# Optimization experiments

Hardware: AMD Instinct MI355X
Metric: run time of the kernel (lower is better)

## Reference

```python
import jax, jax.numpy as jnp
import numpy as np
from jax import lax

B, S, H, W = 16, 5, 64, 64
D, DS, DEPTH, EXPAND, NC = 128, 16, 2, 2, 2


def _ln(x, w, b, eps=1e-5):
    m = x.mean(-1, keepdims=True)
    v = ((x - m) ** 2).mean(-1, keepdims=True)
    return (x - m) / jnp.sqrt(v + eps) * w + b


def _conv2d(x, w, b, stride, pad):
    y = lax.conv_general_dilated(x, w, (stride, stride), [(pad, pad), (pad, pad)],
                                 dimension_numbers=('NCHW', 'OIHW', 'NCHW'))
    return y + b[None, :, None, None]


def _convT2d(x, w, b):
    # torch ConvTranspose2d(k=4, s=2, p=1); w: (Cin, Cout, 4, 4)
    k = jnp.transpose(w[:, :, ::-1, ::-1], (1, 0, 2, 3))
    y = lax.conv_general_dilated(x, k, (1, 1), [(2, 2), (2, 2)], lhs_dilation=(2, 2),
                                 dimension_numbers=('NCHW', 'OIHW', 'NCHW'))
    return y + b[None, :, None, None]


def _dwconv1d(x, w, b):
    # x: [B, L, D]; torch depthwise Conv1d k=4 pad=3 then truncate to L == left-pad 3
    y = lax.conv_general_dilated(x.transpose(0, 2, 1), w, (1,), [(3, 0)],
                                 feature_group_count=w.shape[0],
                                 dimension_numbers=('NCH', 'OIH', 'NCH'))
    return (y + b[None, :, None]).transpose(0, 2, 1)


def _selective_scan(x, ln_w, ln_b, in_w, in_b, x_w, x_b, A_log, Dm, out_w, out_b):
    xn = _ln(x, ln_w, ln_b)
    xz = xn @ in_w.T + in_b
    xp, z = jnp.split(xz, 2, axis=-1)
    xp = jax.nn.silu(xp)
    z = jax.nn.sigmoid(z)
    u = xp @ x_w.T + x_b                        # [B, L, DS]
    a = jnp.exp(-jnp.exp(A_log))[0, 0]          # [DS] decay factor exp(A), A = -exp(A_log)

    def step(h, u_t):
        h = a * h + u_t
        return h, h

    _, hs = lax.scan(step, jnp.zeros((x.shape[0], DS), x.dtype), u.transpose(1, 0, 2))
    hs = hs.transpose(1, 0, 2)                  # [B, L, DS]
    y = (hs @ Dm) * z
    y = y @ out_w.T + out_b                     # dropout is identity at inference
    return x + y


def setup_inputs() -> dict:
    key = jax.random.key(0)
    ks = iter(jax.random.split(key, 64))

    def nrm(shape, scale=0.02):
        return (jax.random.normal(next(ks), shape) * scale).astype(jnp.float32)

    d, ds, hw = D, DS, H * W
    return {
        'x': jax.random.normal(next(ks), (B, S, H, W), dtype=jnp.float32),
        'emb_w': nrm((d, 1, 3, 3), 0.1), 'emb_b': jnp.zeros((d,), jnp.float32),
        'pos_embed': nrm((hw, d)), 'time_embed': nrm((S, d)),
        'blk_ln1_w': jnp.ones((DEPTH, d), jnp.float32), 'blk_ln1_b': jnp.zeros((DEPTH, d), jnp.float32),
        'blk_conv_w': nrm((DEPTH, d, 1, 4), 0.2), 'blk_conv_b': jnp.zeros((DEPTH, d), jnp.float32),
        'blk_sln_w': jnp.ones((DEPTH, d), jnp.float32), 'blk_sln_b': jnp.zeros((DEPTH, d), jnp.float32),
        'blk_A_log': nrm((DEPTH, 1, 1, ds), 0.5),
        'blk_D': nrm((DEPTH, ds, d), 0.1),
        'blk_in_w': nrm((DEPTH, 2 * d, d), 0.05), 'blk_in_b': jnp.zeros((DEPTH, 2 * d), jnp.float32),
        'blk_x_w': nrm((DEPTH, ds, d), 0.05), 'blk_x_b': jnp.zeros((DEPTH, ds), jnp.float32),
        'blk_out_w': nrm((DEPTH, d, d), 0.05), 'blk_out_b': jnp.zeros((DEPTH, d), jnp.float32),
        'blk_ln2_w': jnp.ones((DEPTH, d), jnp.float32), 'blk_ln2_b': jnp.zeros((DEPTH, d), jnp.float32),
        'blk_mlp_w1': nrm((DEPTH, EXPAND * d, d), 0.05), 'blk_mlp_b1': jnp.zeros((DEPTH, EXPAND * d), jnp.float32),
        'blk_mlp_w2': nrm((DEPTH, d, EXPAND * d), 0.05), 'blk_mlp_b2': jnp.zeros((DEPTH, d), jnp.float32),
        'down1_w': nrm((d, d, 3, 3), 0.05), 'down1_b': jnp.zeros((d,), jnp.float32),
        'down2_w': nrm((2 * d, d, 3, 3), 0.05), 'down2_b': jnp.zeros((2 * d,), jnp.float32),
        'bott_w': nrm((2 * d, 2 * d, 3, 3), 0.05), 'bott_b': jnp.zeros((2 * d,), jnp.float32),
        'up1_w': nrm((2 * d, d, 4, 4), 0.05), 'up1_b': jnp.zeros((d,), jnp.float32),
        'up2_w': nrm((2 * d, d, 4, 4), 0.05), 'up2_b': jnp.zeros((d,), jnp.float32),
        'final_w': nrm((NC, 2 * d, 1, 1), 0.05), 'final_b': jnp.zeros((NC,), jnp.float32),
    }


def reference(x, emb_w, emb_b, pos_embed, time_embed,
              blk_ln1_w, blk_ln1_b, blk_conv_w, blk_conv_b,
              blk_sln_w, blk_sln_b, blk_A_log, blk_D,
              blk_in_w, blk_in_b, blk_x_w, blk_x_b, blk_out_w, blk_out_b,
              blk_ln2_w, blk_ln2_b, blk_mlp_w1, blk_mlp_b1, blk_mlp_w2, blk_mlp_b2,
              down1_w, down1_b, down2_w, down2_b, bott_w, bott_b,
              up1_w, up1_b, up2_w, up2_b, final_w, final_b):
    b, s, h, w = x.shape
    # embed all frames at once (linear combination weights: 0.5 each, last frame 1.0)
    e = _conv2d(x.reshape(b * s, 1, h, w), emb_w, emb_b, 1, 1)      # [B*S, D, H, W]
    e = e.reshape(b, s, D, h * w).transpose(0, 1, 3, 2)              # [B, S, HW, D]
    e = e + pos_embed[None, None] + time_embed[:s][None, :, None, :]
    wts = jnp.where(jnp.arange(s) == s - 1, 1.0, 0.5).astype(x.dtype)
    emb = jnp.einsum('bsld,s->bld', e, wts)                          # [B, HW, D]
    for i in range(DEPTH):
        xn = _ln(emb, blk_ln1_w[i], blk_ln1_b[i])
        emb = emb + _dwconv1d(xn, blk_conv_w[i], blk_conv_b[i])
        emb = _selective_scan(emb, blk_sln_w[i], blk_sln_b[i], blk_in_w[i], blk_in_b[i],
                              blk_x_w[i], blk_x_b[i], blk_A_log[i], blk_D[i],
                              blk_out_w[i], blk_out_b[i])
        m = _ln(emb, blk_ln2_w[i], blk_ln2_b[i])
        m = jax.nn.gelu(m @ blk_mlp_w1[i].T + blk_mlp_b1[i], approximate=False)
        emb = emb + (m @ blk_mlp_w2[i].T + blk_mlp_b2[i])
    sp = emb.transpose(0, 2, 1).reshape(b, D, h, w)
    x1 = jax.nn.relu(_conv2d(sp, down1_w, down1_b, 2, 1))
    x2 = jax.nn.relu(_conv2d(x1, down2_w, down2_b, 2, 1))
    x2 = jax.nn.relu(_conv2d(x2, bott_w, bott_b, 1, 1))
    u1 = jax.nn.relu(_convT2d(x2, up1_w, up1_b))
    u1 = jnp.concatenate([u1, x1], axis=1)
    u2 = jax.nn.relu(_convT2d(u1, up2_w, up2_b))
    u2 = jnp.concatenate([u2, sp], axis=1)
    return _conv2d(u2, final_w, final_b, 1, 0)
```

## Files before the change

### kernel.cpp

```cpp
#include <hip/hip_runtime.h>
#include <cmath>

namespace {
constexpr int Bn = 16, Ln = 4096, Dn = 128, DSn = 16;
constexpr int Mtok = Bn * Ln;
constexpr int SLS = 138;
}

typedef short bfx8 __attribute__((ext_vector_type(8)));
typedef float f32x4 __attribute__((ext_vector_type(4)));

static __device__ __forceinline__ ushort f2bf(float f) {
  union { float f; unsigned u; } v; v.f = f;
  unsigned r = v.u + 0x7fff + ((v.u >> 16) & 1);
  return (ushort)(r >> 16);
}
static __device__ __forceinline__ float bf2f(ushort u) {
  union { unsigned u; float f; } v; v.u = ((unsigned)u) << 16;
  return v.f;
}

__global__ void k_prep(const float* __restrict__ inw, const float* __restrict__ outw,
                       const float* __restrict__ m1, const float* __restrict__ m2,
                       const float* __restrict__ xw, const float* __restrict__ cw,
                       const float* __restrict__ d1, const float* __restrict__ d2,
                       const float* __restrict__ bo, const float* __restrict__ u1,
                       const float* __restrict__ u2, ushort* __restrict__ W3,
                       float* __restrict__ CWT) {
  int i = blockIdx.x * 256 + threadIdx.x;
  if (i < 65536) { W3[i] = f2bf(inw[i]); return; }
  if (i < 98304) { W3[i] = f2bf(outw[i - 65536]); return; }
  if (i < 163840) { W3[i] = f2bf(m1[i - 98304]); return; }
  if (i < 229376) { W3[i] = f2bf(m2[i - 163840]); return; }
  if (i < 233472) { W3[i] = f2bf(xw[i - 229376]); return; }
  if (i < 234496) {
    int j = i - 233472; int blk = j >> 9, r = j & 511, d = r >> 2, k = r & 3;
    CWT[blk * 512 + k * 128 + d] = cw[j]; return;
  }
  if (i < 381952) {
    int j = i - 234496; int co = j / (128 * 9); int r = j - co * (128 * 9);
    int ci = r / 9, tap = r - ci * 9;
    W3[233472 + ((size_t)tap * 128 + co) * 128 + ci] = f2bf(d1[j]); return;
  }
  if (i < 676864) {
    int j = i - 381952; int co = j / (128 * 9); int r = j - co * (128 * 9);
    int ci = r / 9, tap = r - ci * 9;
    W3[380928 + ((size_t)tap * 256 + co) * 128 + ci] = f2bf(d2[j]); return;
  }
  if (i < 1266688) {
    int j = i - 676864; int co = j / (256 * 9); int r = j - co * (256 * 9);
    int ci = r / 9, tap = r - ci * 9;
    W3[675840 + ((size_t)tap * 256 + co) * 256 + ci] = f2bf(bo[j]); return;
  }
  if (i < 1790976) {
    int j = i - 1266688; int ci = j / (128 * 16); int r = j - ci * (128 * 16);
    int co = r >> 4, tap = r & 15;
    W3[1265664 + ((size_t)tap * 128 + co) * 256 + ci] = f2bf(u1[j]); return;
  }
  if (i < 2315264) {
    int j = i - 1790976; int ci = j / (128 * 16); int r = j - ci * (128 * 16);
    int co = r >> 4, tap = r & 15;
    W3[1789952 + ((size_t)tap * 128 + co) * 256 + ci] = f2bf(u2[j]); return;
  }
}

__global__ void k_combine(const float* __restrict__ x, float* __restrict__ xc) {
  int i = blockIdx.x * 256 + threadIdx.x;
  int b = i >> 12, p = i & 4095;
  const float* xb = x + (size_t)b * 5 * Ln + p;
  xc[i] = 0.5f * (xb[0] + xb[Ln] + xb[2 * Ln] + xb[3 * Ln]) + xb[4 * Ln];
}

__global__ __launch_bounds__(256) void k_embedln(
    const float* __restrict__ xc, const float* __restrict__ ew, const float* __restrict__ eb,
    const float* __restrict__ pos, const float* __restrict__ te,
    const float* __restrict__ lw, const float* __restrict__ lb,
    ushort* __restrict__ emb, ushort* __restrict__ xn) {
  int tok = blockIdx.x * 8 + (threadIdx.x >> 5);
  int ln = threadIdx.x & 31;
  int b = tok >> 12, l = tok & 4095;
  int h = l >> 6, w = l & 63;
  const float* xb = xc + b * 4096;
  float v[9];
#pragma unroll
  for (int dy = 0; dy < 3; dy++)
#pragma unroll
    for (int dx = 0; dx < 3; dx++) {
      int y = h + dy - 1, xx = w + dx - 1;
      v[dy * 3 + dx] = (y >= 0 && y < 64 && xx >= 0 && xx < 64) ? xb[y * 64 + xx] : 0.f;
    }
  int d0 = ln * 4;
  float o[4]; float s = 0.f, sq = 0.f;
#pragma unroll
  for (int e = 0; e < 4; e++) {
    int d = d0 + e;
    float a = 0.f;
#pragma unroll
    for (int k = 0; k < 9; k++) a += v[k] * ew[d * 9 + k];
    float ts = 0.5f * (te[d] + te[128 + d] + te[256 + d] + te[384 + d]) + te[512 + d];
    float r = a + 3.f * eb[d] + 3.f * pos[l * 128 + d] + ts;
    o[e] = r; s += r; sq += r * r;
  }
  ushort4 eo;
  eo.x = f2bf(o[0]); eo.y = f2bf(o[1]); eo.z = f2bf(o[2]); eo.w = f2bf(o[3]);
  *(ushort4*)(emb + (size_t)tok * 128 + d0) = eo;
#pragma unroll
  for (int off = 16; off; off >>= 1) { s += __shfl_xor(s, off); sq += __shfl_xor(sq, off); }
  float m = s * (1.f / 128.f);
  float var = sq * (1.f / 128.f) - m * m;
  float rs = rsqrtf(var + 1e-5f);
  ushort4 u;
  u.x = f2bf((o[0] - m) * rs * lw[d0 + 0] + lb[d0 + 0]);
  u.y = f2bf((o[1] - m) * rs * lw[d0 + 1] + lb[d0 + 1]);
  u.z = f2bf((o[2] - m) * rs * lw[d0 + 2] + lb[d0 + 2]);
  u.w = f2bf((o[3] - m) * rs * lw[d0 + 3] + lb[d0 + 3]);
  *(ushort4*)(xn + (size_t)tok * 128 + d0) = u;
}

__global__ __launch_bounds__(256) void k_fuse1(
    const ushort* __restrict__ xn1, ushort* __restrict__ emb, ushort* __restrict__ xn2,
    const float* __restrict__ cwT, const float* __restrict__ cb,
    const float* __restrict__ sw, const float* __restrict__ sb) {
  int i = blockIdx.x * 256 + threadIdx.x;
  int g = i & 15, tok = i >> 4, d0 = g * 8, l = tok & 4095;
  const ushort* p = xn1 + (size_t)tok * 128 + d0;
  const bfx8 zf = {0, 0, 0, 0, 0, 0, 0, 0};
  bfx8 v0 = *(const bfx8*)p;
  bfx8 v1 = (l >= 1) ? *(const bfx8*)(p - 128) : zf;
  bfx8 v2 = (l >= 2) ? *(const bfx8*)(p - 256) : zf;
  bfx8 v3 = (l >= 3) ? *(const bfx8*)(p - 384) : zf;
  ushort* ep = emb + (size_t)tok * 128 + d0;
  bfx8 e8 = *(const bfx8*)ep;
  float nv[8]; float s = 0.f, sq = 0.f;
#pragma unroll
  for (int e = 0; e < 8; e++) {
    int d = d0 + e;
    float c = cb[d] + cwT[3 * 128 + d] * bf2f((ushort)v0[e]) + cwT[2 * 128 + d] * bf2f((ushort)v1[e]) +
              cwT[1 * 128 + d] * bf2f((ushort)v2[e]) + cwT[0 * 128 + d] * bf2f((ushort)v3[e]);
    nv[e] = bf2f((ushort)e8[e]) + c;
    s += nv[e]; sq += nv[e] * nv[e];
  }
  bfx8 w8;
#pragma unroll
  for (int e = 0; e < 8; e++) w8[e] = (short)f2bf(nv[e]);
  *(bfx8*)ep = w8;
#pragma unroll
  for (int off = 8; off; off >>= 1) { s += __shfl_xor(s, off); sq += __shfl_xor(sq, off); }
  float m = s * (1.f / 128.f);
  float var = sq * (1.f / 128.f) - m * m;
  float rs = rsqrtf(var + 1e-5f);
  bfx8 r8;
#pragma unroll
  for (int e = 0; e < 8; e++) {
    int d = d0 + e;
    r8[e] = (short)f2bf((nv[e] - m) * rs * sw[d] + sb[d]);
  }
  *(bfx8*)(xn2 + (size_t)tok * 128 + d0) = r8;
}

__global__ __launch_bounds__(256) void k_gemm_xz(
    const ushort* __restrict__ A, const ushort* __restrict__ W, const float* __restrict__ bias,
    ushort* __restrict__ Zu, const ushort* __restrict__ xw, const float* __restrict__ xb,
    float* __restrict__ UT) {
  __shared__ ushort sl[128 * SLS];
  const int t = threadIdx.x;
  const int l = t & 63, wv = t >> 6;
  const int l15 = l & 15, q = l >> 4;
  const int wm = wv >> 1, wn = wv & 1;
  const int m0 = blockIdx.x * 128 + wm * 64;
  const int n0 = blockIdx.y * 128 + wn * 64;
  f32x4 acc[4][4] = {};
  const ushort* Ab = A + (size_t)(m0 + l15) * 128 + q * 8;
  const ushort* Wb = W + (size_t)(n0 + l15) * 128 + q * 8;
#pragma unroll
  for (int k0 = 0; k0 < 128; k0 += 32) {
    bfx8 a[4], b[4];
#pragma unroll
    for (int mf = 0; mf < 4; mf++) a[mf] = *(const bfx8*)(Ab + (size_t)mf * 16 * 128 + k0);
#pragma unroll
    for (int nf = 0; nf < 4; nf++) b[nf] = *(const bfx8*)(Wb + (size_t)nf * 16 * 128 + k0);
#pragma unroll
    for (int mf = 0; mf < 4; mf++)
#pragma unroll
      for (int nf = 0; nf < 4; nf++)
        acc[mf][nf] = __builtin_amdgcn_mfma_f32_16x16x32_bf16(a[mf], b[nf], acc[mf][nf], 0, 0, 0);
  }
  if (blockIdx.y == 1) {
#pragma unroll
    for (int mf = 0; mf < 4; mf++)
#pragma unroll
      for (int nf = 0; nf < 4; nf++) {
        const int col = n0 + nf * 16 + l15;
        const float bb = bias[col];
#pragma unroll
        for (int r = 0; r < 4; r++) {
          const int row = m0 + mf * 16 + q * 4 + r;
          float v = acc[mf][nf][r] + bb;
          Zu[(size_t)row * 128 + col - 128] = f2bf(1.f / (1.f + expf(-v)));
        }
      }
    return;
  }
#pragma unroll
  for (int mf = 0; mf < 4; mf++)
#pragma unroll
    for (int nf = 0; nf < 4; nf++) {
      const int col = wn * 64 + nf * 16 + l15;
      const float bb = bias[col];
#pragma unroll
      for (int r = 0; r < 4; r++) {
        const int rowl = wm * 64 + mf * 16 + q * 4 + r;
        float v = acc[mf][nf][r] + bb;
        sl[rowl * SLS + col] = f2bf(v / (1.f + expf(-v)));
      }
    }
  __syncthreads();
  f32x4 pu[2] = {};
#pragma unroll
  for (int k0 = 0; k0 < 128; k0 += 32) {
    bfx8 bx_ = *(const bfx8*)(xw + l15 * 128 + k0 + q * 8);
#pragma unroll
    for (int mi = 0; mi < 2; mi++) {
      bfx8 a2 = *(const bfx8*)&sl[(wv * 32 + mi * 16 + l15) * SLS + k0 + q * 8];
      pu[mi] = __builtin_amdgcn_mfma_f32_16x16x32_bf16(a2, bx_, pu[mi], 0, 0, 0);
    }
  }
  const float ub = xb[l15];
#pragma unroll
  for (int mi = 0; mi < 2; mi++)
#pragma unroll
    for (int r = 0; r < 4; r++) {
      int token = blockIdx.x * 128 + wv * 32 + mi * 16 + q * 4 + r;
      int b = token >> 12, ll = token & 4095;
      UT[((size_t)(b * 16 + l15)) * 4096 + ll] = pu[mi][r] + ub;
    }
}

__global__ __launch_bounds__(256) void k_gemm_om(
    const ushort* __restrict__ A, const ushort* __restrict__ W1, const float* __restrict__ b1,
    ushort* __restrict__ emb, const float* __restrict__ lw, const float* __restrict__ lb,
    const ushort* __restrict__ W2, const float* __restrict__ b2, ushort* __restrict__ MH) {
  __shared__ ushort sl1[64 * SLS];
  __shared__ float red[2][64][2];
  const int t = threadIdx.x;
  const int l = t & 63, wv = t >> 6;
  const int l15 = l & 15, q = l >> 4;
  const int wm = wv >> 1, wn = wv & 1;
  const int m0 = blockIdx.x * 64;
  const int n0 = wn * 64;
  {
    f32x4 acc[2][4] = {};
    const ushort* Ab = A + (size_t)(m0 + wm * 32 + l15) * 128 + q * 8;
    const ushort* Wb = W1 + (size_t)(n0 + l15) * 128 + q * 8;
#pragma unroll
    for (int k0 = 0; k0 < 128; k0 += 32) {
      bfx8 a[2], b[4];
#pragma unroll
      for (int mf = 0; mf < 2; mf++) a[mf] = *(const bfx8*)(Ab + (size_t)mf * 16 * 128 + k0);
#pragma unroll
      for (int nf = 0; nf < 4; nf++) b[nf] = *(const bfx8*)(Wb + (size_t)nf * 16 * 128 + k0);
#pragma unroll
      for (int mf = 0; mf < 2; mf++)
#pragma unroll
        for (int nf = 0; nf < 4; nf++)
          acc[mf][nf] = __builtin_amdgcn_mfma_f32_16x16x32_bf16(a[mf], b[nf], acc[mf][nf], 0, 0, 0);
    }
    float sv[2][4], qv[2][4];
#pragma unroll
    for (int mf = 0; mf < 2; mf++)
#pragma unroll
      for (int r = 0; r < 4; r++) { sv[mf][r] = 0.f; qv[mf][r] = 0.f; }
#pragma unroll
    for (int mf = 0; mf < 2; mf++)
#pragma unroll
      for (int nf = 0; nf < 4; nf++) {
        const int col = n0 + nf * 16 + l15;
        const float bb = b1[col];
#pragma unroll
        for (int r = 0; r < 4; r++) {
          const int row = m0 + wm * 32 + mf * 16 + q * 4 + r;
          float v = acc[mf][nf][r] + bb + bf2f(emb[(size_t)row * 128 + col]);
          acc[mf][nf][r] = v;
          sv[mf][r] += v; qv[mf][r] += v * v;
        }
      }
#pragma unroll
    for (int mf = 0; mf < 2; mf++)
#pragma unroll
      for (int r = 0; r < 4; r++) {
#pragma unroll
        for (int off = 1; off < 16; off <<= 1) {
          sv[mf][r] += __shfl_xor(sv[mf][r], off);
          qv[mf][r] += __shfl_xor(qv[mf][r], off);
        }
        if (l15 == 0) {
          int rowl = wm * 32 + mf * 16 + q * 4 + r;
          red[0][rowl][wn] = sv[mf][r];
          red[1][rowl][wn] = qv[mf][r];
        }
      }
    __syncthreads();
#pragma unroll
    for (int mf = 0; mf < 2; mf++)
#pragma unroll
      for (int r = 0; r < 4; r++) {
        const int rowl = wm * 32 + mf * 16 + q * 4 + r;
        const int row = m0 + rowl;
        float ts = red[0][rowl][0] + red[0][rowl][1];
        float tq = red[1][rowl][0] + red[1][rowl][1];
        float mm = ts * (1.f / 128.f);
        float var = tq * (1.f / 128.f) - mm * mm;
        float rs = rsqrtf(var + 1e-5f);
#pragma unroll
        for (int nf = 0; nf < 4; nf++) {
          const int col = n0 + nf * 16 + l15;
          float v = acc[mf][nf][r];
          emb[(size_t)row * 128 + col] = f2bf(v);
          sl1[rowl * SLS + col] = f2bf((v - mm) * rs * lw[col] + lb[col]);
        }
      }
  }
  __syncthreads();
  const int rw0 = (wv & 1) * 32;
  const int cw0 = (wv >> 1) * 128;
  f32x4 acc2[2][8] = {};
#pragma unroll
  for (int k0 = 0; k0 < 128; k0 += 32) {
    bfx8 a2[2];
#pragma unroll
    for (int mi = 0; mi < 2; mi++)
      a2[mi] = *(const bfx8*)&sl1[(rw0 + mi * 16 + l15) * SLS + k0 + q * 8];
#pragma unroll
    for (int nf = 0; nf < 8; nf++) {
      bfx8 b2v = *(const bfx8*)(W2 + (size_t)(cw0 + nf * 16 + l15) * 128 + k0 + q * 8);
#pragma unroll
      for (int mi = 0; mi < 2; mi++)
        acc2[mi][nf] = __builtin_amdgcn_mfma_f32_16x16x32_bf16(a2[mi], b2v, acc2[mi][nf], 0, 0, 0);
    }
  }
#pragma unroll
  for (int mi = 0; mi < 2; mi++)
#pragma unroll
    for (int nf = 0; nf < 8; nf++) {
      const int col = cw0 + nf * 16 + l15;
      const float bb = b2[col];
#pragma unroll
      for (int r = 0; r < 4; r++) {
        const int row = m0 + rw0 + mi * 16 + q * 4 + r;
        float v = acc2[mi][nf][r] + bb;
        MH[(size_t)row * 256 + col] = f2bf(0.5f * v * (1.f + erff(v * 0.7071067811865475f)));
      }
    }
}

template <int MODE, int K>
__global__ __launch_bounds__(256) void k_mgemm(const ushort* __restrict__ A, const ushort* __restrict__ W,
                                               const float* __restrict__ bias, void* __restrict__ out2v,
                                               ushort* __restrict__ emb,
                                               const float* __restrict__ lw, const float* __restrict__ lb) {
  __shared__ float red[2][64][2];
  const int t = threadIdx.x;
  const int l = t & 63, wv = t >> 6;
  const int l15 = l & 15, q = l >> 4;
  const int wm = wv >> 1, wn = wv & 1;
  const int m0 = blockIdx.x * 64;
  const int n0 = wn * 64;
  f32x4 acc[2][4] = {};
  const ushort* Ab = A + (size_t)(m0 + wm * 32 + l15) * K + q * 8;
  const ushort* Wb = W + (size_t)(n0 + l15) * K + q * 8;
#pragma unroll
  for (int k0 = 0; k0 < K; k0 += 32) {
    bfx8 a[2], b[4];
#pragma unroll
    for (int mf = 0; mf < 2; mf++) a[mf] = *(const bfx8*)(Ab + (size_t)mf * 16 * K + k0);
#pragma unroll
    for (int nf = 0; nf < 4; nf++) b[nf] = *(const bfx8*)(Wb + (size_t)nf * 16 * K + k0);
#pragma unroll
    for (int mf = 0; mf < 2; mf++)
#pragma unroll
      for (int nf = 0; nf < 4; nf++)
        acc[mf][nf] = __builtin_amdgcn_mfma_f32_16x16x32_bf16(a[mf], b[nf], acc[mf][nf], 0, 0, 0);
  }
  if constexpr (MODE == 4) __syncthreads();
  float sv[2][4], qv[2][4];
#pragma unroll
  for (int mf = 0; mf < 2; mf++)
#pragma unroll
    for (int r = 0; r < 4; r++) { sv[mf][r] = 0.f; qv[mf][r] = 0.f; }
#pragma unroll
  for (int mf = 0; mf < 2; mf++)
#pragma unroll
    for (int nf = 0; nf < 4; nf++) {
      const int col = n0 + nf * 16 + l15;
      const float bb = bias[col];
#pragma unroll
      for (int r = 0; r < 4; r++) {
        const int row = m0 + wm * 32 + mf * 16 + q * 4 + r;
        float v = acc[mf][nf][r] + bb + bf2f(emb[(size_t)row * 128 + col]);
        acc[mf][nf][r] = v;
        sv[mf][r] += v; qv[mf][r] += v * v;
      }
    }
  if constexpr (MODE == 5) {
#pragma unroll
    for (int mf = 0; mf < 2; mf++)
#pragma unroll
      for (int r = 0; r < 4; r++) {
#pragma unroll
        for (int off = 1; off < 16; off <<= 1) {
          sv[mf][r] += __shfl_xor(sv[mf][r], off);
          qv[mf][r] += __shfl_xor(qv[mf][r], off);
        }
        if (l15 == 0) {
          int rowl = wm * 32 + mf * 16 + q * 4 + r;
          red[0][rowl][wn] = sv[mf][r];
          red[1][rowl][wn] = qv[mf][r];
        }
      }
    __syncthreads();
  }
#pragma unroll
  for (int mf = 0; mf < 2; mf++)
#pragma unroll
    for (int r = 0; r < 4; r++) {
      const int rowl = wm * 32 + mf * 16 + q * 4 + r;
      const int row = m0 + rowl;
      float mm = 0.f, rs = 0.f;
      if constexpr (MODE == 5) {
        float ts = red[0][rowl][0] + red[0][rowl][1];
        float tq = red[1][rowl][0] + red[1][rowl][1];
        mm = ts * (1.f / 128.f);
        float var = tq * (1.f / 128.f) - mm * mm;
        rs = rsqrtf(var + 1e-5f);
      }
#pragma unroll
      for (int nf = 0; nf < 4; nf++) {
        const int col = n0 + nf * 16 + l15;
        float v = acc[mf][nf][r];
        emb[(size_t)row * 128 + col] = f2bf(v);
        if constexpr (MODE == 5)
          ((ushort*)out2v)[(size_t)row * 128 + col] = f2bf((v - mm) * rs * lw[col] + lb[col]);
        else
          ((ushort*)out2v)[(size_t)row * 256 + 128 + col] = f2bf(v);
      }
    }
}

__global__ __launch_bounds__(64) void k_scan(const float* __restrict__ UT, float* __restrict__ HST,
                                             const float* __restrict__ A_log) {
  const int b = blockIdx.x >> 4, ds = blockIdx.x & 15;
  const int tid = threadIdx.x;
  const float a = expf(-expf(A_log[ds]));
  const float4* ut4 = (const float4*)(UT + ((size_t)(b * 16 + ds)) * 4096 + tid * 64);
  float r[64];
#pragma unroll
  for (int j4 = 0; j4 < 16; j4++) {
    float4 v = ut4[j4];
    r[j4 * 4 + 0] = v.x; r[j4 * 4 + 1] = v.y; r[j4 * 4 + 2] = v.z; r[j4 * 4 + 3] = v.w;
  }
  float h = 0.f;
#pragma unroll
  for (int j = 0; j < 64; j++) { h = a * h + r[j]; r[j] = h; }
  float a64 = a;
#pragma unroll
  for (int qq = 0; qq < 6; qq++) a64 *= a64;
  float Ac = a64, Bc = h;
#pragma unroll
  for (int off = 1; off < 64; off <<= 1) {
    float Ap = __shfl_up(Ac, off);
    float Bp = __shfl_up(Bc, off);
    if (tid >= off) { Bc = Ac * Bp + Bc; Ac = Ac * Ap; }
  }
  float carry = __shfl_up(Bc, 1);
  if (tid == 0) carry = 0.f;
  float p = a;
#pragma unroll
  for (int j = 0; j < 64; j++) { r[j] += p * carry; p *= a; }
  float4* hb4 = (float4*)(HST + ((size_t)(b * 16 + ds)) * 4096 + tid * 64);
#pragma unroll
  for (int j4 = 0; j4 < 16; j4++) {
    float4 v; v.x = r[j4 * 4 + 0]; v.y = r[j4 * 4 + 1]; v.z = r[j4 * 4 + 2]; v.w = r[j4 * 4 + 3];
    hb4[j4] = v;
  }
}

__global__ __launch_bounds__(256) void k_yb(const float* __restrict__ HST, const float* __restrict__ Dm_,
                                            const ushort* __restrict__ Z, ushort* __restrict__ Y) {
  const int m = blockIdx.x * 2 + (threadIdx.x >> 7);
  const int d = threadIdx.x & 127;
  const int b = m >> 12, l = m & 4095;
  const float* hb = HST + (size_t)b * 16 * Ln + l;
  float acc = 0.f;
#pragma unroll
  for (int s = 0; s < 16; s++) acc += hb[(size_t)s * Ln] * Dm_[s * 128 + d];
  const size_t o = (size_t)m * 128 + d;
  Y[o] = f2bf(acc * bf2f(Z[o]));
}

template <int MODE, int OTH, int OTW, int CIN, int WPB>
__global__ __launch_bounds__(WPB * 64) void k_cv(
    const ushort* __restrict__ in, ushort* __restrict__ out,
    const ushort* __restrict__ wt, const float* __restrict__ bias,
    int Hi, int Wi, int CP, int CO, int CPo, int COo, int Cout,
    int nsp, int nspx, long ibs, long obs) {
  constexpr int ITH = (MODE == 1) ? (2 * OTH + 1) : (OTH + 2);
  constexpr int ITW = (MODE == 1) ? (2 * OTW + 1) : (OTW + 2);
  constexpr int NPIX = ITH * ITW;
  constexpr int SPF = OTH * OTW / 16;
  constexpr int NTAPS = (MODE == 2) ? 4 : 9;
  constexpr int NCH = CIN / 32;
  __shared__ __attribute__((aligned(16))) ushort lds[NPIX * 40];
  const int t = threadIdx.x;
  const int w = t >> 6, l = t & 63;
  const int l15 = l & 15, q = l >> 4;
  const int b = blockIdx.z;
  const int py = (MODE == 2) ? ((int)blockIdx.y >> 1) : 0;
  const int px = (MODE == 2) ? ((int)blockIdx.y & 1) : 0;
  const int cb = blockIdx.x / nsp;
  const int spt = blockIdx.x - cb * nsp;
  const int spy = spt / nspx, spx = spt - spy * nspx;
  const int n0 = cb * (16 * WPB) + w * 16;
  const int y0 = spy * OTH, x0 = spx * OTW;
  const int gy0 = (MODE == 1) ? (2 * y0 - 1) : (y0 - 1);
  const int gx0 = (MODE == 1) ? (2 * x0 - 1) : (x0 - 1);
  const ushort* ib = in + (size_t)b * ibs;
  f32x4 acc[SPF] = {};
  int abase[SPF];
#pragma unroll
  for (int af = 0; af < SPF; af++) {
    int p = af * 16 + l15;
    int ty = p / OTW, tx = p % OTW;
    int sy = (MODE == 1) ? (2 * ty) : ty;
    int sx = (MODE == 1) ? (2 * tx) : tx;
    abase[af] = (sy * ITW + sx) * 40 + q * 8;
  }
  for (int c = 0; c < NCH; c++) {
    const int k0 = c * 32;
    __syncthreads();
    for (int idx = t; idx < NPIX * 4; idx += WPB * 64) {
      int pix = idx >> 2, qq = idx & 3;
      int sy = pix / ITW, sx = pix - sy * ITW;
      int gy = gy0 + sy, gx = gx0 + sx;
      bfx8 v = {0, 0, 0, 0, 0, 0, 0, 0};
      if ((unsigned)gy < (unsigned)Hi && (unsigned)gx < (unsigned)Wi)
        v = *(const bfx8*)(ib + (size_t)(gy * Wi + gx) * CP + CO + k0 + qq * 8);
      *(bfx8*)&lds[pix * 40 + qq * 8] = v;
    }
    __syncthreads();
#pragma unroll
    for (int tap = 0; tap < NTAPS; tap++) {
      const int dy = (MODE == 2) ? (tap >> 1) : (tap / 3);
      const int dx = (MODE == 2) ? (tap & 1) : (tap - (tap / 3) * 3);
      const int tapw = (MODE == 2) ? ((3 - py - 2 * dy) * 4 + (3 - px - 2 * dx)) : tap;
      const int toff = (MODE == 2) ? (((py + dy) * ITW + (px + dx)) * 40)
                                   : ((dy * ITW + dx) * 40);
      bfx8 bv = *(const bfx8*)(wt + ((size_t)tapw * Cout + n0 + l15) * CIN + k0 + q * 8);
#pragma unroll
      for (int af = 0; af < SPF; af++) {
        bfx8 av = *(const bfx8*)&lds[abase[af] + toff];
        acc[af] = __builtin_amdgcn_mfma_f32_16x16x32_bf16(av, bv, acc[af], 0, 0, 0);
      }
    }
  }
  const float bb = bias[n0 + l15];
  ushort* ob = out + (size_t)b * obs + COo + n0 + l15;
#pragma unroll
  for (int af = 0; af < SPF; af++) {
#pragma unroll
    for (int r = 0; r < 4; r++) {
      int p = af * 16 + q * 4 + r;
      int ty = p / OTW, tx = p % OTW;
      int oy, ox, Wo;
      if (MODE == 2) { oy = (y0 + ty) * 2 + py; ox = (x0 + tx) * 2 + px; Wo = Wi * 2; }
      else if (MODE == 1) { oy = y0 + ty; ox = x0 + tx; Wo = Wi / 2; }
      else { oy = y0 + ty; ox = x0 + tx; Wo = Wi; }
      ob[(size_t)(oy * Wo + ox) * CPo] = f2bf(fmaxf(acc[af][r] + bb, 0.f));
    }
  }
}

__global__ __launch_bounds__(256) void k_final3(const ushort* __restrict__ in, const float* __restrict__ w,
                                                const float* __restrict__ bias, float* __restrict__ out) {
  int wid = (blockIdx.x << 2) + (threadIdx.x >> 6);
  int lane = threadIdx.x & 63;
  const ushort* rp = in + (size_t)wid * 256 + lane * 4;
  ushort4 u = *(const ushort4*)rp;
  float f0 = bf2f(u.x), f1 = bf2f(u.y), f2 = bf2f(u.z), f3 = bf2f(u.w);
  float4 w0 = *(const float4*)(w + lane * 4);
  float4 w1 = *(const float4*)(w + 256 + lane * 4);
  float a0 = f0 * w0.x + f1 * w0.y + f2 * w0.z + f3 * w0.w;
  float a1 = f0 * w1.x + f1 * w1.y + f2 * w1.z + f3 * w1.w;
#pragma unroll
  for (int off = 32; off; off >>= 1) { a0 += __shfl_xor(a0, off); a1 += __shfl_xor(a1, off); }
  if (lane == 0) {
    int b = wid >> 12, p = wid & 4095;
    out[(size_t)b * 8192 + p] = a0 + bias[0];
    out[(size_t)b * 8192 + 4096 + p] = a1 + bias[1];
  }
}

extern "C" void kernel_launch(void* const* d_in, const int* in_sizes, int n_in,
                              void* d_out, int out_size, void* d_ws, size_t ws_size,
                              hipStream_t stream) {
  (void)in_sizes; (void)n_in; (void)out_size; (void)ws_size;
  const float* x          = (const float*)d_in[0];
  const float* emb_w      = (const float*)d_in[1];
  const float* emb_b      = (const float*)d_in[2];
  const float* pos_embed  = (const float*)d_in[3];
  const float* time_embed = (const float*)d_in[4];
  const float* blk_ln1_w  = (const float*)d_in[5];
  const float* blk_ln1_b  = (const float*)d_in[6];
  const float* blk_conv_w = (const float*)d_in[7];
  const float* blk_conv_b = (const float*)d_in[8];
  const float* blk_sln_w  = (const float*)d_in[9];
  const float* blk_sln_b  = (const float*)d_in[10];
  const float* blk_A_log  = (const float*)d_in[11];
  const float* blk_D      = (const float*)d_in[12];
  const float* blk_in_w   = (const float*)d_in[13];
  const float* blk_in_b   = (const float*)d_in[14];
  const float* blk_x_w    = (const float*)d_in[15];
  const float* blk_x_b    = (const float*)d_in[16];
  const float* blk_out_w  = (const float*)d_in[17];
  const float* blk_out_b  = (const float*)d_in[18];
  const float* blk_ln2_w  = (const float*)d_in[19];
  const float* blk_ln2_b  = (const float*)d_in[20];
  const float* blk_mlp_w1 = (const float*)d_in[21];
  const float* blk_mlp_b1 = (const float*)d_in[22];
  const float* blk_mlp_w2 = (const float*)d_in[23];
  const float* blk_mlp_b2 = (const float*)d_in[24];
  const float* down1_w    = (const float*)d_in[25];
  const float* down1_b    = (const float*)d_in[26];
  const float* down2_w    = (const float*)d_in[27];
  const float* down2_b    = (const float*)d_in[28];
  const float* bott_w     = (const float*)d_in[29];
  const float* bott_b     = (const float*)d_in[30];
  const float* up1_w      = (const float*)d_in[31];
  const float* up1_b      = (const float*)d_in[32];
  const float* up2_w      = (const float*)d_in[33];
  const float* up2_b      = (const float*)d_in[34];
  const float* final_w    = (const float*)d_in[35];
  const float* final_b    = (const float*)d_in[36];

  float* ws = (float*)d_ws;
  constexpr size_t F = 1u << 20;
  ushort* EMBh = (ushort*)ws;
  ushort* XN1 = (ushort*)(ws + 8 * F);
  ushort* XN2 = XN1 + 8 * F;
  ushort* MH  = (ushort*)(ws + 16 * F);
  ushort* Zu  = (ushort*)(ws + 24 * F);
  ushort* W3  = (ushort*)(ws + 28 * F);
  float* Ubuf = ws + 32 * F;
  float* HST  = ws + 33 * F;

  ushort* Wi  = W3;
  ushort* Wo  = W3 + 65536;
  ushort* Wm1 = W3 + 98304;
  ushort* Wm2 = W3 + 163840;
  ushort* Wx  = W3 + 229376;
  ushort* Wd1 = W3 + 233472;
  ushort* Wd2 = W3 + 380928;
  ushort* Wb9 = W3 + 675840;
  ushort* Wu1 = W3 + 1265664;
  ushort* Wu2 = W3 + 1789952;
  float*  CWT = (float*)(W3 + 2314240);

  k_prep<<<9044, 256, 0, stream>>>(blk_in_w, blk_out_w, blk_mlp_w1, blk_mlp_w2, blk_x_w,
                                   blk_conv_w, down1_w, down2_w, bott_w, up1_w, up2_w, W3, CWT);
  k_combine<<<256, 256, 0, stream>>>(x, Ubuf);
  k_embedln<<<8192, 256, 0, stream>>>(Ubuf, emb_w, emb_b, pos_embed, time_embed,
                                      blk_ln1_w, blk_ln1_b, EMBh, XN1);

  ushort* U2C = MH;
  for (int i = 0; i < 2; i++) {
    k_fuse1<<<4096, 256, 0, stream>>>(XN1, EMBh, XN2, CWT + i * 512, blk_conv_b + i * Dn,
                                      blk_sln_w + i * Dn, blk_sln_b + i * Dn);
    k_gemm_xz<<<dim3(512, 2), 256, 0, stream>>>(XN2, Wi + i * 32768, blk_in_b + i * 256,
                                                Zu, Wx + i * 2048, blk_x_b + i * DSn, Ubuf);
    k_scan<<<256, 64, 0, stream>>>(Ubuf, HST, blk_A_log + i * DSn);
    k_yb<<<32768, 256, 0, stream>>>(HST, blk_D + i * DSn * Dn, Zu, XN2);
    k_gemm_om<<<1024, 256, 0, stream>>>(XN2, Wo + i * 16384, blk_out_b + i * Dn,
                                        EMBh, blk_ln2_w + i * Dn, blk_ln2_b + i * Dn,
                                        Wm1 + i * 32768, blk_mlp_b1 + i * 256, MH);
    if (i == 0)
      k_mgemm<5, 256><<<1024, 256, 0, stream>>>(MH, Wm2 + i * 32768, blk_mlp_b2 + i * Dn,
                                                XN1, EMBh, blk_ln1_w + Dn, blk_ln1_b + Dn);
    else
      k_mgemm<4, 256><<<1024, 256, 0, stream>>>(MH, Wm2 + i * 32768, blk_mlp_b2 + i * Dn,
                                                U2C, EMBh, nullptr, nullptr);
  }

  ushort* U1C = XN1;
  ushort* X2b = XN1 + 8388608;
  ushort* X3b = X2b + 1048576;

  k_cv<1, 8, 8, 128, 4><<<dim3(2 * 16, 1, 16), 256, 0, stream>>>(
      U2C, U1C, Wd1, down1_b, 64, 64, 256, 128, 256, 128, 128,
      16, 4, 64L * 64 * 256, 32L * 32 * 256);
  k_cv<1, 8, 8, 128, 2><<<dim3(8 * 4, 1, 16), 128, 0, stream>>>(
      U1C, X2b, Wd2, down2_b, 32, 32, 256, 128, 256, 0, 256,
      4, 2, 32L * 32 * 256, 16L * 16 * 256);
  k_cv<0, 8, 8, 256, 2><<<dim3(8 * 4, 1, 16), 128, 0, stream>>>(
      X2b, X3b, Wb9, bott_b, 16, 16, 256, 0, 256, 0, 256,
      4, 2, 16L * 16 * 256, 16L * 16 * 256);
  k_cv<2, 8, 16, 256, 2><<<dim3(4 * 2, 4, 16), 128, 0, stream>>>(
      X3b, U1C, Wu1, up1_b, 16, 16, 256, 0, 256, 0, 128,
      2, 1, 16L * 16 * 256, 32L * 32 * 256);
  k_cv<2, 16, 16, 256, 4><<<dim3(2 * 4, 4, 16), 256, 0, stream>>>(
      U1C, U2C, Wu2, up2_b, 32, 32, 256, 0, 256, 0, 128,
      4, 2, 32L * 32 * 256, 64L * 64 * 256);

  k_final3<<<16384, 256, 0, stream>>>(U2C, final_w, final_b, (float*)d_out);
}
```

Before: 508.8 us.

## Prefetch residual before GEMM, retile MLP2 warps, use tanh-style GELU approximation

The residual emb values are loaded into registers before the MFMA loop in both fused GEMM kernels, so their latency overlaps with the matrix compute instead of stalling the epilogue. The second GEMM in k_gemm_om is retiled so each wave covers all 64 rows and 64 columns, which reuses W2 fragments across more rows. The exact erf GELU is replaced with a sigmoid-based tanh approximation, which is cheaper but numerically deviates from the exact GELU the reference uses. The prefetch adds register pressure.

```diff
diff --git a/kernel.cpp b/kernel.cpp
--- a/kernel.cpp
+++ b/kernel.cpp
@@ -18,6 +18,10 @@
 static __device__ __forceinline__ float bf2f(ushort u) {
   union { unsigned u; float f; } v; v.u = ((unsigned)u) << 16;
   return v.f;
+}
+static __device__ __forceinline__ float gelu_fast(float x) {
+  float u = x * (1.5957691216f + 0.07135481f * x * x);
+  return x / (1.f + expf(-u));
 }
 
 __global__ void k_prep(const float* __restrict__ inw, const float* __restrict__ outw,
@@ -249,6 +253,14 @@
   const int m0 = blockIdx.x * 64;
   const int n0 = wn * 64;
   {
+    ushort epre[2][4][4];
+#pragma unroll
+    for (int mf = 0; mf < 2; mf++)
+#pragma unroll
+      for (int nf = 0; nf < 4; nf++)
+#pragma unroll
+        for (int r = 0; r < 4; r++)
+          epre[mf][nf][r] = emb[(size_t)(m0 + wm * 32 + mf * 16 + q * 4 + r) * 128 + n0 + nf * 16 + l15];
     f32x4 acc[2][4] = {};
     const ushort* Ab = A + (size_t)(m0 + wm * 32 + l15) * 128 + q * 8;
     const ushort* Wb = W1 + (size_t)(n0 + l15) * 128 + q * 8;
@@ -278,8 +290,7 @@
         const float bb = b1[col];
 #pragma unroll
         for (int r = 0; r < 4; r++) {
-          const int row = m0 + wm * 32 + mf * 16 + q * 4 + r;
-          float v = acc[mf][nf][r] + bb + bf2f(emb[(size_t)row * 128 + col]);
+          float v = acc[mf][nf][r] + bb + bf2f(epre[mf][nf][r]);
           acc[mf][nf][r] = v;
           sv[mf][r] += v; qv[mf][r] += v * v;
         }
@@ -321,34 +332,33 @@
       }
   }
   __syncthreads();
-  const int rw0 = (wv & 1) * 32;
-  const int cw0 = (wv >> 1) * 128;
-  f32x4 acc2[2][8] = {};
+  const int cw0 = wv * 64;
+  f32x4 acc2[4][4] = {};
 #pragma unroll
   for (int k0 = 0; k0 < 128; k0 += 32) {
-    bfx8 a2[2];
-#pragma unroll
-    for (int mi = 0; mi < 2; mi++)
-      a2[mi] = *(const bfx8*)&sl1[(rw0 + mi * 16 + l15) * SLS + k0 + q * 8];
-#pragma unroll
-    for (int nf = 0; nf < 8; nf++) {
+    bfx8 a2[4];
+#pragma unroll
+    for (int mi = 0; mi < 4; mi++)
+      a2[mi] = *(const bfx8*)&sl1[(mi * 16 + l15) * SLS + k0 + q * 8];
+#pragma unroll
+    for (int nf = 0; nf < 4; nf++) {
       bfx8 b2v = *(const bfx8*)(W2 + (size_t)(cw0 + nf * 16 + l15) * 128 + k0 + q * 8);
 #pragma unroll
-      for (int mi = 0; mi < 2; mi++)
+      for (int mi = 0; mi < 4; mi++)
         acc2[mi][nf] = __builtin_amdgcn_mfma_f32_16x16x32_bf16(a2[mi], b2v, acc2[mi][nf], 0, 0, 0);
     }
   }
 #pragma unroll
-  for (int mi = 0; mi < 2; mi++)
-#pragma unroll
-    for (int nf = 0; nf < 8; nf++) {
+  for (int mi = 0; mi < 4; mi++)
+#pragma unroll
+    for (int nf = 0; nf < 4; nf++) {
       const int col = cw0 + nf * 16 + l15;
       const float bb = b2[col];
 #pragma unroll
       for (int r = 0; r < 4; r++) {
-        const int row = m0 + rw0 + mi * 16 + q * 4 + r;
+        const int row = m0 + mi * 16 + q * 4 + r;
         float v = acc2[mi][nf][r] + bb;
-        MH[(size_t)row * 256 + col] = f2bf(0.5f * v * (1.f + erff(v * 0.7071067811865475f)));
+        MH[(size_t)row * 256 + col] = f2bf(gelu_fast(v));
       }
     }
 }
@@ -365,6 +375,14 @@
   const int wm = wv >> 1, wn = wv & 1;
   const int m0 = blockIdx.x * 64;
   const int n0 = wn * 64;
+  ushort epre[2][4][4];
+#pragma unroll
+  for (int mf = 0; mf < 2; mf++)
+#pragma unroll
+    for (int nf = 0; nf < 4; nf++)
+#pragma unroll
+      for (int r = 0; r < 4; r++)
+        epre[mf][nf][r] = emb[(size_t)(m0 + wm * 32 + mf * 16 + q * 4 + r) * 128 + n0 + nf * 16 + l15];
   f32x4 acc[2][4] = {};
   const ushort* Ab = A + (size_t)(m0 + wm * 32 + l15) * K + q * 8;
   const ushort* Wb = W + (size_t)(n0 + l15) * K + q * 8;
@@ -395,8 +413,7 @@
       const float bb = bias[col];
 #pragma unroll
       for (int r = 0; r < 4; r++) {
-        const int row = m0 + wm * 32 + mf * 16 + q * 4 + r;
-        float v = acc[mf][nf][r] + bb + bf2f(emb[(size_t)row * 128 + col]);
+        float v = acc[mf][nf][r] + bb + bf2f(epre[mf][nf][r]);
         acc[mf][nf][r] = v;
         sv[mf][r] += v; qv[mf][r] += v * v;
       }
```

Measured after the change: 485.1 us. 4.7% less time.
